# Kernel tuning notes

Measured on AMD Instinct MI355X. Metric: run time of the kernel, lower is better.

Reference implementation:

```python
import jax, jax.numpy as jnp
import numpy as np

B, S, N, H, V = 8, 512, 32, 256, 100001
NEG = -1e9
SLOPE = 0.2  # LeakyReLU negative slope


def setup_inputs() -> dict:
    key = jax.random.key(0)
    k1, k2, k3, k4, k5 = jax.random.split(key, 5)
    node_ids = jax.random.randint(k1, (B, S), 0, V)
    neighs = jax.random.randint(k2, (B, S, N), 0, V)
    mask = jax.random.randint(k3, (B, S, N, 1), 0, 2).astype(jnp.int32)
    emb_table = jax.random.normal(k4, (V, H), dtype=jnp.float32) * 0.02
    a_w = jax.random.normal(k5, (2 * H, 1), dtype=jnp.float32) * (1.0 / np.sqrt(2 * H))
    a_b = jnp.zeros((1,), dtype=jnp.float32)
    return {"node_ids": node_ids, "neighs": neighs, "mask": mask,
            "emb_table": emb_table, "a_w": a_w, "a_b": a_b}


def reference(node_ids, neighs, mask, emb_table, a_w, a_b):
    # Gather embeddings
    src = emb_table[node_ids][:, :, None, :]          # [B,S,1,H]
    nbr = emb_table[neighs]                           # [B,S,N,H]
    neigh_embs = jnp.concatenate([src, nbr], axis=2)  # [B,S,N+1,H] (self + neighbors)
    # Concat src with each candidate -> [B,S,N+1,2H]
    src_rep = jnp.broadcast_to(src, neigh_embs.shape)
    embs = jnp.concatenate([src_rep, neigh_embs], axis=-1)
    # Tiny linear (2H -> 1) + LeakyReLU(0.2)
    z = embs @ a_w + a_b                              # [B,S,N+1,1]
    att = jnp.where(z > 0, z, SLOPE * z)
    # Mask neighbor slots (self at index 0 is never masked)
    att = att.at[:, :, 1:].add(mask.astype(att.dtype) * NEG)
    w = jax.nn.softmax(att, axis=2)                   # [B,S,N+1,1]
    # Weighted aggregate: w^T @ neigh_embs
    out = jnp.sum(w * neigh_embs, axis=2)             # [B,S,H]
    return out
```

## Files before the change

### kernel.cpp

```cpp
#include <hip/hip_runtime.h>
#include <math.h>


constexpr int H    = 256;
constexpr int NN   = 32;
constexpr int C    = NN + 1;
constexpr int WPB  = 8;
constexpr int JMAX = (C + WPB - 1) / WPB;
constexpr float SLOPE = 0.2f;

__device__ __forceinline__ float wave_sum(float v) {
#pragma unroll
  for (int off = 32; off > 0; off >>= 1)
    v += __shfl_xor(v, off, 64);
  return v;
}

__global__ __launch_bounds__(512, 6) void gat_kernel(
    const int*   __restrict__ node_ids,
    const int*   __restrict__ neighs,
    const int*   __restrict__ mask,
    const float* __restrict__ emb,
    const float* __restrict__ a_w,
    const float* __restrict__ a_b,
    float*       __restrict__ out)
{
  __shared__ int    sidx[WPB][64];
  __shared__ float  smx[WPB], ssum[WPB];
  __shared__ float4 sacc[WPB][64];

  const int pos  = blockIdx.x;
  const int wv   = threadIdx.x >> 6;
  const int lane = threadIdx.x & 63;
  const int l4   = lane << 2;

  bool active = false;
  int  my     = 0;
  if (lane == 0) {
    my = node_ids[pos];
    active = true;
  } else if (lane <= NN) {
    my     = neighs[pos * NN + lane - 1];
    active = (mask[pos * NN + lane - 1] == 0);
  }
  const unsigned long long bal = __ballot(active);
  const int K = (int)__popcll(bal);
  if (active)
    sidx[wv][(int)__popcll(bal & ((1ull << lane) - 1ull))] = my;
  const int cidx = sidx[wv][lane];
  const int swv  = __builtin_amdgcn_readfirstlane(wv);

  const float4 aw1 = *(const float4*)(a_w + l4);
  const float4 aw2 = *(const float4*)(a_w + H + l4);
  const float  ab  = a_b[0];
  const float4* __restrict__ embv = (const float4*)emb;

  const int    iself = __builtin_amdgcn_readlane(cidx, 0);
  const float4 es    = embv[(size_t)iself * (H / 4) + lane];

  float4 buf[JMAX];
#pragma unroll
  for (int j = 0; j < JMAX; ++j) {
    const int c = swv + WPB * j;
    if (c < K) {
      const int ic = __builtin_amdgcn_readlane(cidx, c);
      buf[j] = embv[(size_t)ic * (H / 4) + lane];
    }
  }

  const float zsrc = wave_sum(es.x * aw1.x + es.y * aw1.y +
                              es.z * aw1.z + es.w * aw1.w);

  float  m = -1e30f, s = 0.f;
  float4 acc = {0.f, 0.f, 0.f, 0.f};
#pragma unroll
  for (int j = 0; j < JMAX; ++j) {
    const int c = swv + WPB * j;
    if (c < K) {
      const float4 cur = buf[j];
      const float  p   = wave_sum(cur.x * aw2.x + cur.y * aw2.y +
                                  cur.z * aw2.z + cur.w * aw2.w);
      const float z = zsrc + p + ab;
      const float a = (z > 0.f) ? z : SLOPE * z;
      const float mnew  = fmaxf(m, a);
      const float scale = __expf(m - mnew);
      const float pr    = __expf(a - mnew);
      s = s * scale + pr;
      acc.x = acc.x * scale + pr * cur.x;
      acc.y = acc.y * scale + pr * cur.y;
      acc.z = acc.z * scale + pr * cur.z;
      acc.w = acc.w * scale + pr * cur.w;
      m = mnew;
    }
  }

  sacc[wv][lane] = acc;
  if (lane == 0) { smx[wv] = m; ssum[wv] = s; }
  __syncthreads();

  if (wv == 0) {
    float M = -1e30f;
#pragma unroll
    for (int w = 0; w < WPB; ++w) M = fmaxf(M, smx[w]);
    float  S = 0.f;
    float4 o = {0.f, 0.f, 0.f, 0.f};
#pragma unroll
    for (int w = 0; w < WPB; ++w) {
      const float f = __expf(smx[w] - M);
      S += ssum[w] * f;
      const float4 a = sacc[w][lane];
      o.x += f * a.x; o.y += f * a.y; o.z += f * a.z; o.w += f * a.w;
    }
    const float inv = 1.f / S;
    o.x *= inv; o.y *= inv; o.z *= inv; o.w *= inv;
    *(float4*)(out + (size_t)pos * H + l4) = o;
  }
}

extern "C" void kernel_launch(void* const* d_in, const int* in_sizes, int n_in,
                              void* d_out, int out_size, void* d_ws, size_t ws_size,
                              hipStream_t stream) {
  const int*   node_ids = (const int*)d_in[0];
  const int*   neighs   = (const int*)d_in[1];
  const int*   mask     = (const int*)d_in[2];
  const float* emb      = (const float*)d_in[3];
  const float* a_w      = (const float*)d_in[4];
  const float* a_b      = (const float*)d_in[5];
  float*       out      = (float*)d_out;

  const int npos = in_sizes[0];
  gat_kernel<<<npos, 512, 0, stream>>>(node_ids, neighs, mask, emb, a_w, a_b,
                                       out);
}
```

Before: 155.3 us.

## Halve waves per block and batch wave reductions before a two-pass softmax

The block shrinks from 8 waves to 4, so each wave handles up to 9 candidate rows instead of 5. All per-candidate dot products and the self term are reduced together through one interleaved shuffle butterfly, which exposes independent shuffles. The online softmax is replaced by a max pass followed by an exp/accumulate pass, removing the rescale exps. The cost is more registers per wave and fewer waves in flight per position, with launch bounds changed to match.

```diff
diff --git a/kernel.cpp b/kernel.cpp
--- a/kernel.cpp
+++ b/kernel.cpp
@@ -5,18 +5,12 @@
 constexpr int H    = 256;
 constexpr int NN   = 32;
 constexpr int C    = NN + 1;
-constexpr int WPB  = 8;
+constexpr int WPB  = 4;
 constexpr int JMAX = (C + WPB - 1) / WPB;
+constexpr int NR   = JMAX + 1;
 constexpr float SLOPE = 0.2f;
 
-__device__ __forceinline__ float wave_sum(float v) {
-#pragma unroll
-  for (int off = 32; off > 0; off >>= 1)
-    v += __shfl_xor(v, off, 64);
-  return v;
-}
-
-__global__ __launch_bounds__(512, 6) void gat_kernel(
+__global__ __launch_bounds__(256, 5) void gat_kernel(
     const int*   __restrict__ node_ids,
     const int*   __restrict__ neighs,
     const int*   __restrict__ mask,
@@ -68,29 +62,50 @@
     }
   }
 
-  const float zsrc = wave_sum(es.x * aw1.x + es.y * aw1.y +
-                              es.z * aw1.z + es.w * aw1.w);
+  float red[NR];
+  red[0] = es.x * aw1.x + es.y * aw1.y + es.z * aw1.z + es.w * aw1.w;
+#pragma unroll
+  for (int j = 0; j < JMAX; ++j) {
+    const int c = swv + WPB * j;
+    red[j + 1] = 0.f;
+    if (c < K) {
+      const float4 cur = buf[j];
+      red[j + 1] = cur.x * aw2.x + cur.y * aw2.y +
+                   cur.z * aw2.z + cur.w * aw2.w;
+    }
+  }
+#pragma unroll
+  for (int off = 32; off > 0; off >>= 1) {
+#pragma unroll
+    for (int t = 0; t < NR; ++t)
+      red[t] += __shfl_xor(red[t], off, 64);
+  }
+  const float zsrc = red[0];
 
-  float  m = -1e30f, s = 0.f;
+  float aj[JMAX];
+  float m = -1e30f;
+#pragma unroll
+  for (int j = 0; j < JMAX; ++j) {
+    const int c = swv + WPB * j;
+    if (c < K) {
+      const float z = zsrc + red[j + 1] + ab;
+      aj[j] = (z > 0.f) ? z : SLOPE * z;
+      m = fmaxf(m, aj[j]);
+    }
+  }
+  float  s = 0.f;
   float4 acc = {0.f, 0.f, 0.f, 0.f};
 #pragma unroll
   for (int j = 0; j < JMAX; ++j) {
     const int c = swv + WPB * j;
     if (c < K) {
+      const float pr = __expf(aj[j] - m);
+      s += pr;
       const float4 cur = buf[j];
-      const float  p   = wave_sum(cur.x * aw2.x + cur.y * aw2.y +
-                                  cur.z * aw2.z + cur.w * aw2.w);
-      const float z = zsrc + p + ab;
-      const float a = (z > 0.f) ? z : SLOPE * z;
-      const float mnew  = fmaxf(m, a);
-      const float scale = __expf(m - mnew);
-      const float pr    = __expf(a - mnew);
-      s = s * scale + pr;
-      acc.x = acc.x * scale + pr * cur.x;
-      acc.y = acc.y * scale + pr * cur.y;
-      acc.z = acc.z * scale + pr * cur.z;
-      acc.w = acc.w * scale + pr * cur.w;
-      m = mnew;
+      acc.x += pr * cur.x;
+      acc.y += pr * cur.y;
+      acc.z += pr * cur.z;
+      acc.w += pr * cur.w;
     }
   }
 
@@ -99,9 +114,7 @@
   __syncthreads();
 
   if (wv == 0) {
-    float M = -1e30f;
-#pragma unroll
-    for (int w = 0; w < WPB; ++w) M = fmaxf(M, smx[w]);
+    const float M = fmaxf(fmaxf(smx[0], smx[1]), fmaxf(smx[2], smx[3]));
     float  S = 0.f;
     float4 o = {0.f, 0.f, 0.f, 0.f};
 #pragma unroll
@@ -129,6 +142,6 @@
   float*       out      = (float*)d_out;
 
   const int npos = in_sizes[0];
-  gat_kernel<<<npos, 512, 0, stream>>>(node_ids, neighs, mask, emb, a_w, a_b,
+  gat_kernel<<<npos, 256, 0, stream>>>(node_ids, neighs, mask, emb, a_w, a_b,
                                        out);
 }
```

After: 152.0 us. -2.1%, faster.
